# Optimization experiments

Measured on AMD Instinct MI355X. Metric: run time of the kernel, lower is better.

Reference implementation:

```python
import jax, jax.numpy as jnp
import numpy as np

ALPHA = 0.2  # LeakyReLU negative slope
NEG_INF = -9e15


def setup_inputs() -> dict:
    key = jax.random.key(0)
    k1, k2, k3, k4 = jax.random.split(key, 4)
    B, T, N, F_in, F_out = 8, 8, 1024, 64, 64
    h = jax.random.normal(k1, (B, T, N, F_in), dtype=jnp.float32)
    adj = jax.random.randint(k2, (B, T, N, N), 0, 2, dtype=jnp.int32)
    # xavier_uniform with gain=1.414
    def xavier(k, shape, gain=1.414):
        fan_in, fan_out = shape[0], shape[1]
        bound = gain * np.sqrt(6.0 / (fan_in + fan_out))
        return jax.random.uniform(k, shape, jnp.float32, -bound, bound)
    W = xavier(k3, (F_in, F_out))
    a = xavier(k4, (2 * F_out, 1))
    return {"h": h, "adj": adj, "W": W, "a": a}


def reference(h, adj, W, a):
    # h: [B,T,N,F_in], adj: [B,T,N,N], W: [F_in,F_out], a: [2*F_out,1]
    F_out = W.shape[1]
    Wh = h @ W  # [B,T,N,F_out]
    a1 = a[:F_out, 0]   # source half
    a2 = a[F_out:, 0]   # target half
    s1 = Wh @ a1        # [B,T,N]
    s2 = Wh @ a2        # [B,T,N]
    # e[...,i,j] = LeakyReLU(s1_i + s2_j)  == original concat-linear score
    e = jax.nn.leaky_relu(s1[..., :, None] + s2[..., None, :], negative_slope=ALPHA)
    att = jnp.where(adj > 0, e, NEG_INF)
    att = jax.nn.softmax(att, axis=-1)  # [B,T,N,N]
    # dropout omitted: reference runs in eval mode (p only active in training)
    h_prime = att @ Wh  # [B,T,N,F_out]
    return jax.nn.elu(h_prime)  # concat=True path
```

## Files before the change

### kernel.cpp

```cpp
#include <hip/hip_runtime.h>

#define NN 1024
#define FF 64
#define NBT 64
#define INV_LN2 1.44269504088896f

typedef float f32x4 __attribute__((ext_vector_type(4)));
typedef short s16x8 __attribute__((ext_vector_type(8)));

__device__ __forceinline__ short f2bf(float f) {
    unsigned u = __builtin_bit_cast(unsigned, f);
    u = (u + 0x7FFFu + ((u >> 16) & 1u)) >> 16;
    return (short)u;
}

__global__ __launch_bounds__(256) void k1(const float* __restrict__ h,
                                          const float* __restrict__ W,
                                          const float* __restrict__ a,
                                          short* __restrict__ WhT,
                                          float* __restrict__ s1g,
                                          float* __restrict__ s2g) {
    __shared__ float Wl[64 * 64];
    __shared__ float al[128];
    __shared__ float s1sh[128], s2sh[128];
    const int blk = blockIdx.x;
    const int bt = blk >> 3;
    const int rbase = (blk & 7) * 128;
    const int t = threadIdx.x;

    for (int i = t; i < 1024; i += 256)
        ((f32x4*)Wl)[i] = ((const f32x4*)W)[i];
    if (t < 32) ((f32x4*)al)[t] = ((const f32x4*)a)[t];
    __syncthreads();

    const int row = rbase + (t & 127);
    const int half = t >> 7;
    const float* hrow = h + ((size_t)bt * NN + row) * FF;
    float hv[64];
#pragma unroll
    for (int i = 0; i < 16; i++)
        ((f32x4*)hv)[i] = ((const f32x4*)hrow)[i];

    float s1 = 0.f, s2 = 0.f;
    short* wt = WhT + (size_t)bt * FF * NN + row;
#pragma unroll
    for (int cgi = 0; cgi < 8; cgi++) {
        const int cg = half * 8 + cgi;
        f32x4 acc = {0.f, 0.f, 0.f, 0.f};
#pragma unroll
        for (int k = 0; k < 64; k++) {
            f32x4 w4 = ((const f32x4*)Wl)[k * 16 + cg];
            acc += hv[k] * w4;
        }
        const int c0 = cg * 4;
        s1 += acc.x * al[c0] + acc.y * al[c0 + 1] + acc.z * al[c0 + 2] + acc.w * al[c0 + 3];
        s2 += acc.x * al[64 + c0] + acc.y * al[64 + c0 + 1] + acc.z * al[64 + c0 + 2] + acc.w * al[64 + c0 + 3];
        wt[(size_t)(c0 + 0) * NN] = f2bf(acc.x);
        wt[(size_t)(c0 + 1) * NN] = f2bf(acc.y);
        wt[(size_t)(c0 + 2) * NN] = f2bf(acc.z);
        wt[(size_t)(c0 + 3) * NN] = f2bf(acc.w);
    }
    if (half == 1) { s1sh[t & 127] = s1; s2sh[t & 127] = s2; }
    __syncthreads();
    if (half == 0) {
        s1g[bt * NN + row] = (s1 + s1sh[t]) * INV_LN2;
        s2g[bt * NN + row] = (s2 + s2sh[t]) * INV_LN2;
    }
}

__global__ __launch_bounds__(256, 4) void k2(const int* __restrict__ adj,
                                             const short* __restrict__ WhT,
                                             const float* __restrict__ s1g,
                                             const float* __restrict__ s2g,
                                             float* __restrict__ out) {
    __shared__ __align__(16) short Pa[2][64 * 40];
    __shared__ __align__(16) short Pw[2][64 * 40];
    __shared__ float s2l[NN];

    const int bxl = blockIdx.x;
    const int bx = (bxl & 7) * 128 + (bxl >> 3);
    const int bt = bx >> 4;
    const int ibase = (bx & 15) * 64;
    const int t = threadIdx.x;

    ((f32x4*)s2l)[t] = ((const f32x4*)(s2g + (size_t)bt * NN))[t];

    const int r = t >> 2;
    const int jc = (t & 3) * 8;
    const float s1v = s1g[bt * NN + ibase + r];

    const int* adjp = adj + ((size_t)bt * NN + ibase + r) * NN + jc;
    const short* whp = WhT + (size_t)bt * FF * NN + (size_t)r * NN + jc;

    const int wv = t >> 6;
    const int l = t & 63;
    const int m = l & 15;
    const int q = l >> 4;
    const int foff = (wv * 16 + m) * 40 + q * 8;
    const int boff0 = (0 * 16 + m) * 40 + q * 8;
    const int boff1 = (1 * 16 + m) * 40 + q * 8;
    const int boff2 = (2 * 16 + m) * 40 + q * 8;
    const int boff3 = (3 * 16 + m) * 40 + q * 8;

    f32x4 acc0 = {0.f, 0.f, 0.f, 0.f};
    f32x4 acc1 = {0.f, 0.f, 0.f, 0.f};
    f32x4 acc2 = {0.f, 0.f, 0.f, 0.f};
    f32x4 acc3 = {0.f, 0.f, 0.f, 0.f};
    f32x4 accR = {0.f, 0.f, 0.f, 0.f};
    const s16x8 ones = {0x3F80, 0x3F80, 0x3F80, 0x3F80, 0x3F80, 0x3F80, 0x3F80, 0x3F80};

    int4 ca0 = *(const int4*)(adjp);
    int4 ca1 = *(const int4*)(adjp + 4);
    int4 ca2 = *(const int4*)(adjp + 32);
    int4 ca3 = *(const int4*)(adjp + 36);
    int4 cw  = *(const int4*)(whp);

    __syncthreads();

    for (int pp = 0; pp < 16; pp++) {
        const int nb = (pp < 15 ? pp + 1 : 15) * 64;
        int4 na0 = *(const int4*)(adjp + nb);
        int4 na1 = *(const int4*)(adjp + nb + 4);
        int4 na2 = *(const int4*)(adjp + nb + 32);
        int4 na3 = *(const int4*)(adjp + nb + 36);

        int4 nw;
#pragma unroll
        for (int u = 0; u < 2; u++) {
            const int jt = pp * 2 + u;
            const int b = jt & 1;
            const int4 xa0 = (u == 0) ? ca0 : ca2;
            const int4 xa1 = (u == 0) ? ca1 : ca3;

            int aj[8] = {xa0.x, xa0.y, xa0.z, xa0.w, xa1.x, xa1.y, xa1.z, xa1.w};
            f32x4 s2a = *(const f32x4*)&s2l[jt * 32 + jc];
            f32x4 s2b = *(const f32x4*)&s2l[jt * 32 + jc + 4];
            float sv[8] = {s2a.x, s2a.y, s2a.z, s2a.w, s2b.x, s2b.y, s2b.z, s2b.w};
            s16x8 pbv;
#pragma unroll
            for (int k = 0; k < 8; k++) {
                float e = s1v + sv[k];
                e = fmaxf(e, 0.2f * e);
                e = fminf(e, 86.f);
                float p = (aj[k] > 0) ? exp2f(e) : 0.f;
                pbv[k] = f2bf(p);
            }
            *(s16x8*)&Pa[b][r * 40 + jc] = pbv;
            *(int4*)&Pw[b][r * 40 + jc] = cw;
            __syncthreads();

            const int jn = (jt < 31 ? jt + 1 : 31) * 32;
            nw = *(const int4*)(whp + jn);

            s16x8 af = *(const s16x8*)&Pa[b][foff];
            acc0 = __builtin_amdgcn_mfma_f32_16x16x32_bf16(af, *(const s16x8*)&Pw[b][boff0], acc0, 0, 0, 0);
            acc1 = __builtin_amdgcn_mfma_f32_16x16x32_bf16(af, *(const s16x8*)&Pw[b][boff1], acc1, 0, 0, 0);
            acc2 = __builtin_amdgcn_mfma_f32_16x16x32_bf16(af, *(const s16x8*)&Pw[b][boff2], acc2, 0, 0, 0);
            acc3 = __builtin_amdgcn_mfma_f32_16x16x32_bf16(af, *(const s16x8*)&Pw[b][boff3], acc3, 0, 0, 0);
            accR = __builtin_amdgcn_mfma_f32_16x16x32_bf16(af, ones, accR, 0, 0, 0);

            cw = nw;
        }
        ca0 = na0; ca1 = na1; ca2 = na2; ca3 = na3;
    }

    float rinv[4];
#pragma unroll
    for (int e = 0; e < 4; e++)
        rinv[e] = accR[e] > 0.f ? 1.f / accR[e] : 0.f;

    float* outp = out + ((size_t)bt * NN + ibase + wv * 16 + q * 4) * FF + m;
#pragma unroll
    for (int e = 0; e < 4; e++) {
        float v0 = acc0[e] * rinv[e];
        float v1 = acc1[e] * rinv[e];
        float v2 = acc2[e] * rinv[e];
        float v3 = acc3[e] * rinv[e];
        v0 = v0 > 0.f ? v0 : expm1f(v0);
        v1 = v1 > 0.f ? v1 : expm1f(v1);
        v2 = v2 > 0.f ? v2 : expm1f(v2);
        v3 = v3 > 0.f ? v3 : expm1f(v3);
        float* o = outp + (size_t)e * FF;
        o[0]  = v0;
        o[16] = v1;
        o[32] = v2;
        o[48] = v3;
    }
}

extern "C" void kernel_launch(void* const* d_in, const int* in_sizes, int n_in,
                              void* d_out, int out_size, void* d_ws, size_t ws_size,
                              hipStream_t stream) {
    const float* h  = (const float*)d_in[0];
    const int*  adj = (const int*)d_in[1];
    const float* W  = (const float*)d_in[2];
    const float* a  = (const float*)d_in[3];
    float* out = (float*)d_out;

    short* WhT = (short*)d_ws;
    float* s1  = (float*)((char*)d_ws + (size_t)NBT * FF * NN * 2);
    float* s2  = s1 + NBT * NN;

    k1<<<512, 256, 0, stream>>>(h, W, a, WhT, s1, s2);
    k2<<<1024, 256, 0, stream>>>(adj, WhT, s1, s2, out);
}
```

Before: 409.5 us.

## Replace shared-memory P/Wh staging with cross-lane shuffles and direct B loads

Each wave now computes the attention probabilities for its own 16 rows and rearranges them into the MFMA A-operand layout with __shfl, so the shared-memory P buffer and the per-step __syncthreads go away. Wh^T B-fragments are loaded from global memory straight into registers by every wave instead of being staged once per block in LDS. This removes block-wide barriers and LDS traffic from the inner loop. In exchange, each wave issues its own Wh loads (four times the global/L2 traffic for Wh) and holds more live registers.

```diff
diff --git a/kernel.cpp b/kernel.cpp
--- a/kernel.cpp
+++ b/kernel.cpp
@@ -73,8 +73,6 @@
                                              const float* __restrict__ s1g,
                                              const float* __restrict__ s2g,
                                              float* __restrict__ out) {
-    __shared__ __align__(16) short Pa[2][64 * 40];
-    __shared__ __align__(16) short Pw[2][64 * 40];
     __shared__ float s2l[NN];
 
     const int bxl = blockIdx.x;
@@ -82,25 +80,21 @@
     const int bt = bx >> 4;
     const int ibase = (bx & 15) * 64;
     const int t = threadIdx.x;
-
-    ((f32x4*)s2l)[t] = ((const f32x4*)(s2g + (size_t)bt * NN))[t];
-
-    const int r = t >> 2;
-    const int jc = (t & 3) * 8;
-    const float s1v = s1g[bt * NN + ibase + r];
-
-    const int* adjp = adj + ((size_t)bt * NN + ibase + r) * NN + jc;
-    const short* whp = WhT + (size_t)bt * FF * NN + (size_t)r * NN + jc;
-
     const int wv = t >> 6;
     const int l = t & 63;
+
+    ((f32x4*)s2l)[t] = ((const f32x4*)(s2g + (size_t)bt * NN))[t];
+
+    const int sr = wv * 16 + (l >> 2);
+    const int jc = (l & 3) * 8;
+    const float s1v = s1g[bt * NN + ibase + sr];
+    const int* adjp = adj + ((size_t)bt * NN + ibase + sr) * NN + jc;
+
     const int m = l & 15;
     const int q = l >> 4;
-    const int foff = (wv * 16 + m) * 40 + q * 8;
-    const int boff0 = (0 * 16 + m) * 40 + q * 8;
-    const int boff1 = (1 * 16 + m) * 40 + q * 8;
-    const int boff2 = (2 * 16 + m) * 40 + q * 8;
-    const int boff3 = (3 * 16 + m) * 40 + q * 8;
+    const int srcLane = ((l & 15) << 2) | (l >> 4);
+
+    const short* whp = WhT + (size_t)bt * FF * NN + (size_t)m * NN + q * 8;
 
     f32x4 acc0 = {0.f, 0.f, 0.f, 0.f};
     f32x4 acc1 = {0.f, 0.f, 0.f, 0.f};
@@ -113,7 +107,10 @@
     int4 ca1 = *(const int4*)(adjp + 4);
     int4 ca2 = *(const int4*)(adjp + 32);
     int4 ca3 = *(const int4*)(adjp + 36);
-    int4 cw  = *(const int4*)(whp);
+    s16x8 cb0 = *(const s16x8*)(whp);
+    s16x8 cb1 = *(const s16x8*)(whp + 16 * NN);
+    s16x8 cb2 = *(const s16x8*)(whp + 32 * NN);
+    s16x8 cb3 = *(const s16x8*)(whp + 48 * NN);
 
     __syncthreads();
 
@@ -124,13 +121,17 @@
         int4 na2 = *(const int4*)(adjp + nb + 32);
         int4 na3 = *(const int4*)(adjp + nb + 36);
 
-        int4 nw;
 #pragma unroll
         for (int u = 0; u < 2; u++) {
             const int jt = pp * 2 + u;
-            const int b = jt & 1;
             const int4 xa0 = (u == 0) ? ca0 : ca2;
             const int4 xa1 = (u == 0) ? ca1 : ca3;
+
+            const int jn = (jt < 31 ? jt + 1 : 31) * 32;
+            s16x8 nb0 = *(const s16x8*)(whp + jn);
+            s16x8 nb1 = *(const s16x8*)(whp + 16 * NN + jn);
+            s16x8 nb2 = *(const s16x8*)(whp + 32 * NN + jn);
+            s16x8 nb3 = *(const s16x8*)(whp + 48 * NN + jn);
 
             int aj[8] = {xa0.x, xa0.y, xa0.z, xa0.w, xa1.x, xa1.y, xa1.z, xa1.w};
             f32x4 s2a = *(const f32x4*)&s2l[jt * 32 + jc];
@@ -145,21 +146,21 @@
                 float p = (aj[k] > 0) ? exp2f(e) : 0.f;
                 pbv[k] = f2bf(p);
             }
-            *(s16x8*)&Pa[b][r * 40 + jc] = pbv;
-            *(int4*)&Pw[b][r * 40 + jc] = cw;
-            __syncthreads();
-
-            const int jn = (jt < 31 ? jt + 1 : 31) * 32;
-            nw = *(const int4*)(whp + jn);
-
-            s16x8 af = *(const s16x8*)&Pa[b][foff];
-            acc0 = __builtin_amdgcn_mfma_f32_16x16x32_bf16(af, *(const s16x8*)&Pw[b][boff0], acc0, 0, 0, 0);
-            acc1 = __builtin_amdgcn_mfma_f32_16x16x32_bf16(af, *(const s16x8*)&Pw[b][boff1], acc1, 0, 0, 0);
-            acc2 = __builtin_amdgcn_mfma_f32_16x16x32_bf16(af, *(const s16x8*)&Pw[b][boff2], acc2, 0, 0, 0);
-            acc3 = __builtin_amdgcn_mfma_f32_16x16x32_bf16(af, *(const s16x8*)&Pw[b][boff3], acc3, 0, 0, 0);
+
+            union { s16x8 v; int d[4]; } pu, au;
+            pu.v = pbv;
+#pragma unroll
+            for (int w = 0; w < 4; w++)
+                au.d[w] = __shfl(pu.d[w], srcLane);
+            const s16x8 af = au.v;
+
+            acc0 = __builtin_amdgcn_mfma_f32_16x16x32_bf16(af, cb0, acc0, 0, 0, 0);
+            acc1 = __builtin_amdgcn_mfma_f32_16x16x32_bf16(af, cb1, acc1, 0, 0, 0);
+            acc2 = __builtin_amdgcn_mfma_f32_16x16x32_bf16(af, cb2, acc2, 0, 0, 0);
+            acc3 = __builtin_amdgcn_mfma_f32_16x16x32_bf16(af, cb3, acc3, 0, 0, 0);
             accR = __builtin_amdgcn_mfma_f32_16x16x32_bf16(af, ones, accR, 0, 0, 0);
 
-            cw = nw;
+            cb0 = nb0; cb1 = nb1; cb2 = nb2; cb3 = nb3;
         }
         ca0 = na0; ca1 = na1; ca2 = na2; ca3 = na3;
     }
```

After: 411.8 us. Within noise of the previous version (+0.6%).
